# Kernel tuning notes

Measured on AMD Instinct MI355X. Metric: run time of the kernel, lower is better.

## Reference

```python
import jax, jax.numpy as jnp
import numpy as np

BIG = 1e10  # sentinel for geodesic-style padding in min/max morphology


def _cross_neighbors(x, pad_val):
    # x: [B,1,H,W]; gather center + 4-connected neighbors (cross structuring element)
    xp = jnp.pad(x, ((0, 0), (0, 0), (1, 1), (1, 1)), constant_values=pad_val)
    c = xp[:, :, 1:-1, 1:-1]
    u = xp[:, :, :-2, 1:-1]
    d = xp[:, :, 2:, 1:-1]
    l = xp[:, :, 1:-1, :-2]
    r = xp[:, :, 1:-1, 2:]
    return jnp.stack([c, u, d, l, r], axis=0)  # [5,B,1,H,W]


def opening_cross(x):
    # morphology opening = dilation(erosion(x)) with binary cross kernel
    er = jnp.min(_cross_neighbors(x, BIG), axis=0)
    return jnp.max(_cross_neighbors(er, -BIG), axis=0)


def torch_norm(x):
    mn = jnp.min(x)
    mx = jnp.max(x)
    return (x - mn) / (mx - mn + 1e-10)


def binarize(x):
    return jnp.where(x >= 0.5, jnp.float32(1.0), jnp.float32(0.0))


def connected_components(mask, num_iterations=150):
    # kornia.contrib.connected_components: init labels = flat pixel index on
    # foreground, then iterate 3x3 max-pool label propagation restricted to mask.
    B, C, H, W = mask.shape
    init = jnp.arange(B * C * H * W, dtype=jnp.float32).reshape(B, C, H, W) * mask
    fg = mask != 0

    def maxpool3(x):
        return jax.lax.reduce_window(
            x, -jnp.inf, jax.lax.max,
            window_dimensions=(1, 1, 3, 3), window_strides=(1, 1, 1, 1),
            padding='SAME')

    def body(i, out):
        return jnp.where(fg, maxpool3(out), out)

    return jax.lax.fori_loop(0, num_iterations, body, init)


def count_unique(x):
    # jit-compatible torch.unique(...).size()[0]: sort then count transitions.
    # Label values <= B*H*W < 2^24 so float32 comparisons are exact.
    s = jnp.sort(x.reshape(-1))
    return jnp.float32(1.0) + jnp.sum(s[1:] != s[:-1]).astype(jnp.float32)


def setup_inputs() -> dict:
    key = jax.random.key(0)
    k1, k2 = jax.random.split(key)
    img = jax.random.uniform(k1, (4, 1, 1024, 1024), dtype=jnp.float32)
    lab = jax.random.uniform(k2, (4, 1, 1024, 1024), dtype=jnp.float32)
    return {"img": img, "lab": lab}


def reference(img, lab):
    img = binarize(torch_norm(opening_cross(img)))
    lab = binarize(torch_norm(opening_cross(lab)))
    ccs = count_unique(connected_components(img, 150))
    ccsg = count_unique(connected_components(lab, 150))
    numSg = jnp.sum(lab)  # count_nonzero of binary mask
    C = jnp.abs(ccsg - ccs) / numSg
    return jnp.mean(C)
```

## Files before the change

kernel.cpp:

```cpp
#include <hip/hip_runtime.h>
#include <stdint.h>

#define WW 1024
#define HH 1024
#define NB 4
#define HW (HH * WW)
#define NPIX (NB * HW)
#define NT 4096
#define INVALID 0xFFFFFFFFu
#define RS 8


__device__ __forceinline__ void do_open_strip(const float* __restrict__ in,
                                              float* __restrict__ out,
                                              int strip, uint32_t* S,
                                              float2* __restrict__ mmslot) {
    int b  = strip >> 7;
    int y0 = (strip & 127) * RS;
    int t  = threadIdx.x;
    float* sx = (float*)S;
    float* sw = (float*)S + 2580;
    float* smin = (float*)S + 5160;
    float* smax = (float*)S + 5164;
    const float4* inb = (const float4*)(in + (size_t)b * HW);
    float4* outb      = (float4*)(out + (size_t)b * HW);

    float4 A[RS + 4];
    #pragma unroll
    for (int j = 0; j < RS + 4; j++) {
        int iy = y0 - 2 + j;
        if (iy >= 0 && iy < HH) A[j] = inb[iy * 256 + t];
        else A[j] = make_float4(1e10f, 1e10f, 1e10f, 1e10f);
    }
    #pragma unroll
    for (int rr = 0; rr < RS + 2; rr++) { sx[rr * 258 + t + 1] = A[rr + 1].x; sw[rr * 258 + t + 1] = A[rr + 1].w; }
    if (t < RS + 2) { sw[t * 258 + 0] = 1e10f; sx[t * 258 + 257] = 1e10f; }
    __syncthreads();

    float4 E[RS + 2];
    #pragma unroll
    for (int rr = 0; rr < RS + 2; rr++) {
        int ey = y0 - 1 + rr;
        float lw = sw[rr * 258 + t], rw = sx[rr * 258 + t + 2];
        float4 v = A[rr + 1];
        float hx = fminf(fminf(lw, v.x), v.y);
        float hy = fminf(fminf(v.x, v.y), v.z);
        float hz = fminf(fminf(v.y, v.z), v.w);
        float hw = fminf(fminf(v.z, v.w), rw);
        float4 e;
        e.x = fminf(hx, fminf(A[rr].x, A[rr + 2].x));
        e.y = fminf(hy, fminf(A[rr].y, A[rr + 2].y));
        e.z = fminf(hz, fminf(A[rr].z, A[rr + 2].z));
        e.w = fminf(hw, fminf(A[rr].w, A[rr + 2].w));
        if (ey < 0 || ey >= HH) e = make_float4(-1e10f, -1e10f, -1e10f, -1e10f);
        E[rr] = e;
    }
    __syncthreads();

    #pragma unroll
    for (int d = 0; d < RS; d++) { sx[d * 258 + t + 1] = E[d + 1].x; sw[d * 258 + t + 1] = E[d + 1].w; }
    if (t < RS) { sw[t * 258 + 0] = -1e10f; sx[t * 258 + 257] = -1e10f; }
    __syncthreads();

    float lmin = __uint_as_float(0x7F800000u);
    float lmax = 0.0f;
    #pragma unroll
    for (int d = 0; d < RS; d++) {
        float lw = sw[d * 258 + t], rw = sx[d * 258 + t + 2];
        float4 v = E[d + 1];
        float hx = fmaxf(fmaxf(lw, v.x), v.y);
        float hy = fmaxf(fmaxf(v.x, v.y), v.z);
        float hz = fmaxf(fmaxf(v.y, v.z), v.w);
        float hw = fmaxf(fmaxf(v.z, v.w), rw);
        float4 o;
        o.x = fmaxf(hx, fmaxf(E[d].x, E[d + 2].x));
        o.y = fmaxf(hy, fmaxf(E[d].y, E[d + 2].y));
        o.z = fmaxf(hz, fmaxf(E[d].z, E[d + 2].z));
        o.w = fmaxf(hw, fmaxf(E[d].w, E[d + 2].w));
        outb[(y0 + d) * 256 + t] = o;
        lmin = fminf(lmin, fminf(fminf(o.x, o.y), fminf(o.z, o.w)));
        lmax = fmaxf(lmax, fmaxf(fmaxf(o.x, o.y), fmaxf(o.z, o.w)));
    }
    for (int off = 32; off > 0; off >>= 1) {
        lmin = fminf(lmin, __shfl_down(lmin, off));
        lmax = fmaxf(lmax, __shfl_down(lmax, off));
    }
    if ((t & 63) == 0) { smin[t >> 6] = lmin; smax[t >> 6] = lmax; }
    __syncthreads();
    if (t == 0) {
        float m0 = fminf(fminf(smin[0], smin[1]), fminf(smin[2], smin[3]));
        float m1 = fmaxf(fmaxf(smax[0], smax[1]), fmaxf(smax[2], smax[3]));
        *mmslot = make_float2(m0, m1);
    }
}

__device__ __forceinline__ float calc_thr(float mn, float mx) {
    float denom = (mx - mn) + 1e-10f;
    uint32_t lo = 0, hi = 0x7F800000u;
    while (lo < hi) {
        uint32_t mid = (lo + hi) >> 1;
        float q = (__uint_as_float(mid) - mn) / denom;
        if (q >= 0.5f) hi = mid; else lo = mid + 1;
    }
    return __uint_as_float(lo);
}

__device__ __forceinline__ uint32_t lload(uint32_t* lp, uint32_t x) {
    return __hip_atomic_load(&lp[x], __ATOMIC_RELAXED, __HIP_MEMORY_SCOPE_WORKGROUP);
}
__device__ __forceinline__ uint32_t lfind(uint32_t* lp, uint32_t x) {
    uint32_t p = lload(lp, x);
    while (p != x) {
        uint32_t gp = lload(lp, p);
        if (gp != p)
            __hip_atomic_store(&lp[x], gp, __ATOMIC_RELAXED, __HIP_MEMORY_SCOPE_WORKGROUP);
        x = p; p = gp;
    }
    return x;
}
__device__ uint32_t lunion(uint32_t* lp, uint32_t a, uint32_t b) {
    uint32_t ra = lfind(lp, a), rb = lfind(lp, b);
    while (ra != rb) {
        uint32_t hi = ra > rb ? ra : rb;
        uint32_t lo = ra ^ rb ^ hi;
        uint32_t old = atomicCAS(&lp[lo], lo, hi);
        if (old == lo) return 1;
        ra = lfind(lp, old);
        rb = lfind(lp, hi);
    }
    return 0;
}
__device__ __forceinline__ int run_len(uint32_t bits) {
    return (int)__builtin_ctzll(~(uint64_t)bits);
}

__device__ void do_ccl_tile(const float* __restrict__ opened, uint8_t* __restrict__ desc,
                            uint32_t* __restrict__ parent, uint32_t* __restrict__ zt,
                            int bank, int tile, int L,
                            uint32_t* M, uint32_t* LP, uint32_t* SM,
                            float thr, uint32_t* pkslot) {
    int b  = tile >> 10;
    int tt = tile & 1023;
    int ty0 = (tt >> 5) << 5;
    int tx0 = (tt & 31) << 5;
    uint32_t base = (uint32_t)b * HW + (uint32_t)ty0 * WW + tx0;

    #pragma unroll
    for (int q = 0; q < 2; q++) {
        uint32_t u = (uint32_t)L + 64u * q;
        ((uint4*)LP)[u] = make_uint4(4*u, 4*u+1, 4*u+2, 4*u+3);
        ((uint4*)SM)[u] = make_uint4(INVALID, INVALID, INVALID, INVALID);
    }

    int r8 = L >> 3, c8 = (L & 7) << 2;
    uint32_t fgcnt = 0;
    #pragma unroll
    for (int q = 0; q < 4; q++) {
        int rr = r8 + 8 * q;
        float4 v = *(const float4*)(opened + base + (uint32_t)rr * WW + c8);
        uint32_t pb = (v.x >= thr ? 1u : 0u) | (v.y >= thr ? 2u : 0u)
                    | (v.z >= thr ? 4u : 0u) | (v.w >= thr ? 8u : 0u);
        fgcnt += __popc(pb);
        uint32_t part = pb << c8;
        part |= __shfl_xor(part, 1, 8);
        part |= __shfl_xor(part, 2, 8);
        part |= __shfl_xor(part, 4, 8);
        if ((L & 7) == 0) M[rr] = part;
    }
    __syncthreads();

    int r = L >> 1, h = L & 1;
    uint32_t rowm = M[r];
    uint32_t fstarts = rowm & ~(rowm << 1);
    uint32_t halfsel = 0xFFFFu << (16 * h);
    uint32_t starts = fstarts & halfsel;
    uint32_t runs = __popc(starts);
    uint32_t links = 0;
    if (r > 0 && starts) {
        uint32_t up = M[r - 1];
        uint32_t upstarts = up & ~(up << 1);
        uint32_t w0 = starts;
        while (w0) {
            int lx = __builtin_ctz(w0); w0 &= w0 - 1;
            int e = lx + run_len(rowm >> lx) - 1;
            int lo = lx ? lx - 1 : 0;
            int hi = (e >= 31) ? 31 : e + 1;
            uint32_t hm = (hi == 31) ? 0xFFFFFFFFu : ((1u << (hi + 1)) - 1u);
            uint32_t w = up & hm & ~((1u << lo) - 1u);
            uint32_t repA = ((uint32_t)r << 4) + __popc(fstarts & ((2u << e) - 1u)) - 1u;
            while (w) {
                int xs = __builtin_ctz(w);
                int xe = xs + run_len(up >> xs) - 1;
                uint32_t repB = (((uint32_t)r - 1) << 4)
                              + __popc(upstarts & ((2u << xe) - 1u)) - 1u;
                links += lunion(LP, repA, repB);
                w = (xe >= 31) ? 0u : (w & ~((1u << (xe + 1)) - 1u));
            }
        }
    }
    __syncthreads();

    if (tile == 0 && L == 0)
        zt[bank] = ((rowm & 1u) && !(rowm & 2u) && LP[0] == 0u) ? 1u : 0u;

    uint32_t rk[2]; bool fgk[2];
    #pragma unroll
    for (int j = 0; j < 2; j++) {
        int k = 2 * L + j;
        int li = (k < 32) ? k
               : (k < 64) ? (31 * 32 + (k - 32))
               : (k < 96) ? ((k - 64) << 5)
                          : (((k - 96) << 5) + 31);
        int ly = li >> 5, lx = li & 31;
        uint32_t rm = M[ly];
        bool f = (rm >> lx) & 1u;
        fgk[j] = f;
        if (f) {
            int e = lx + run_len(rm >> lx) - 1;
            uint32_t rst = rm & ~(rm << 1);
            uint32_t lbl = ((uint32_t)ly << 4) + __popc(rst & ((2u << e) - 1u)) - 1u;
            rk[j] = lfind(LP, lbl);
            atomicMin(&SM[rk[j]], (uint32_t)k);
        }
    }
    __syncthreads();

    uint32_t nodebase = (uint32_t)tile << 7;
    uint32_t d2 = 0;
    #pragma unroll
    for (int j = 0; j < 2; j++) {
        int k = 2 * L + j;
        uint32_t sb = 0xFFu;
        if (fgk[j]) {
            uint32_t s = SM[rk[j]];
            sb = s;
            if (s == (uint32_t)k) parent[nodebase + k] = nodebase + k;
        }
        d2 |= sb << (8 * j);
    }
    ((uint16_t*)desc)[((uint32_t)tile << 6) + L] = (uint16_t)d2;

    uint32_t pk = (fgcnt << 20) | (runs << 10) | links;
    for (int off = 32; off > 0; off >>= 1) pk += __shfl_down(pk, off);
    if (L == 0) *pkslot = pk;
    __syncthreads();
}

__device__ __forceinline__ uint32_t pload(uint32_t* P, uint32_t x) {
    return __hip_atomic_load(&P[x], __ATOMIC_RELAXED, __HIP_MEMORY_SCOPE_AGENT);
}
__device__ __forceinline__ uint32_t uf_find(uint32_t* P, uint32_t x) {
    uint32_t p = pload(P, x);
    while (p != x) {
        uint32_t gp = pload(P, p);
        if (gp != p)
            __hip_atomic_store(&P[x], gp, __ATOMIC_RELAXED, __HIP_MEMORY_SCOPE_AGENT);
        x = p; p = gp;
    }
    return x;
}
__device__ uint32_t uf_union(uint32_t* P, uint32_t a, uint32_t b) {
    uint32_t ra = uf_find(P, a);
    uint32_t rb = uf_find(P, b);
    while (ra != rb) {
        uint32_t hi = ra > rb ? ra : rb;
        uint32_t lo = ra ^ rb ^ hi;
        uint32_t old = atomicCAS(&P[lo], lo, hi);
        if (old == lo) return 1;
        ra = uf_find(P, old);
        rb = uf_find(P, hi);
    }
    return 0;
}

__global__ void k_open2(const float* __restrict__ img, const float* __restrict__ lab,
                        float* __restrict__ op0, float* __restrict__ op1,
                        float2* __restrict__ mm) {
    __shared__ uint32_t S[5168];
    int bank = blockIdx.x >> 9;
    do_open_strip(bank ? lab : img, bank ? op1 : op0,
                  blockIdx.x & 511, S, &mm[blockIdx.x]);
}

__global__ __launch_bounds__(256, 8) void k_ccl2(const float* __restrict__ op0,
                                                 const float* __restrict__ op1,
                                                 uint8_t* __restrict__ d0,
                                                 uint8_t* __restrict__ d1,
                                                 uint32_t* __restrict__ p0,
                                                 uint32_t* __restrict__ p1,
                                                 const float2* __restrict__ mm,
                                                 unsigned long long* __restrict__ fcs,
                                                 uint32_t* __restrict__ zt) {
    __shared__ uint32_t S[4240];
    int bank = blockIdx.x >> 10;
    int wave = threadIdx.x >> 6, L = threadIdx.x & 63;
    if (blockIdx.x == 0 && threadIdx.x == 0) zt[2] = 0;
    {
        const float2* mb = mm + (bank << 9);
        float2 u = mb[threadIdx.x];
        float2 v = mb[threadIdx.x + 256];
        float mn = fminf(u.x, v.x), mx = fmaxf(u.y, v.y);
        for (int off = 32; off > 0; off >>= 1) {
            mn = fminf(mn, __shfl_down(mn, off));
            mx = fmaxf(mx, __shfl_down(mx, off));
        }
        float* sf = (float*)(S + 4228);
        if (L == 0) { sf[wave] = mn; sf[4 + wave] = mx; }
    }
    __syncthreads();
    float* sf = (float*)(S + 4228);
    float mnA = fminf(fminf(sf[0], sf[1]), fminf(sf[2], sf[3]));
    float mxA = fmaxf(fmaxf(sf[4], sf[5]), fmaxf(sf[6], sf[7]));
    float thr = calc_thr(mnA, mxA);
    uint32_t* M = S + wave * 1056;
    int tile = ((blockIdx.x & 1023) << 2) + wave;
    do_ccl_tile(bank ? op1 : op0, bank ? d1 : d0, bank ? p1 : p0, zt, bank,
                tile, L, M, M + 32, M + 544, thr, &S[4224 + wave]);
    if (threadIdx.x == 0) {
        uint32_t fg = 0, comp = 0;
        #pragma unroll
        for (int w = 0; w < 4; w++) {
            uint32_t pk = S[4224 + w];
            fg   += pk >> 20;
            comp += ((pk >> 10) & 1023u) - (pk & 1023u);
        }
        fcs[blockIdx.x] = ((unsigned long long)comp << 32) | fg;
    }
}

__global__ __launch_bounds__(256) void k_border(const uint8_t* __restrict__ desc0,
                                                const uint8_t* __restrict__ desc1,
                                                uint32_t* __restrict__ parent0,
                                                uint32_t* __restrict__ parent1,
                                                unsigned long long* __restrict__ fcs,
                                                uint32_t* __restrict__ lks,
                                                uint32_t* __restrict__ zt,
                                                float* __restrict__ out) {
    __shared__ unsigned long long Q[800];
    __shared__ uint32_t qn;
    __shared__ uint32_t SW[6];
    __shared__ unsigned long long SB[8];
    __shared__ uint32_t SL[8];
    int inb  = blockIdx.x >> 10;
    int wave = threadIdx.x >> 6, L = threadIdx.x & 63;
    int tile = ((blockIdx.x & 1023) << 2) + wave;
    const uint8_t* desc = inb ? desc1 : desc0;
    uint32_t* parent = inb ? parent1 : parent0;

    if (threadIdx.x == 0) qn = 0;
    __syncthreads();

    {
        int tt = tile & 1023;
        int tyy = tt >> 5, txx = tt & 31;
        const uint8_t* dT = desc + ((uint32_t)tile << 7);
        uint32_t nT = (uint32_t)tile << 7;

        bool east  = (L < 32);
        int  x     = L & 31;
        bool valid = east ? (txx < 31) : (tyy < 31);
        int  tP    = east ? (tile + 1) : (tile + 32);
        uint32_t nP = (uint32_t)tP << 7;
        uint32_t sA = (uint32_t)dT[(east ? 96 : 32) + x];
        const uint8_t* dP = desc + (((uint32_t)tP << 7) + (east ? 64u : 0u));
        uint32_t t = valid ? (uint32_t)dP[x] : 0xFFu;

        uint32_t tp1  = __shfl(t,  L + 1);
        uint32_t tm1  = __shfl(t,  L - 1);
        uint32_t sAp1 = __shfl(sA, L + 1);
        uint32_t sAm1 = __shfl(sA, L - 1);

        if (valid && sA != 0xFFu) {
            uint32_t a = nT + sA;
            if (t != 0xFFu && !(x > 0 && sAm1 == sA && tm1 == t)) {
                uint32_t i = atomicAdd(&qn, 1u);
                Q[i] = ((unsigned long long)a << 32) | (nP + t);
            }
            if (x < 31 && tp1 != 0xFFu && tp1 != t && sAp1 != sA) {
                uint32_t i = atomicAdd(&qn, 1u);
                Q[i] = ((unsigned long long)a << 32) | (nP + tp1);
            }
            if (x > 0 && tm1 != 0xFFu && tm1 != t && sAm1 != sA) {
                uint32_t i = atomicAdd(&qn, 1u);
                Q[i] = ((unsigned long long)a << 32) | (nP + tm1);
            }
        }
        if (L == 0 && tyy < 31 && txx < 31) {
            int tSE = tile + 33;
            uint32_t sB = dT[63];
            uint32_t sQ = desc[((uint32_t)tSE << 7)];
            if (sB != 0xFFu && sQ != 0xFFu) {
                uint32_t i = atomicAdd(&qn, 1u);
                Q[i] = ((unsigned long long)(nT + sB) << 32) | (((uint32_t)tSE << 7) + sQ);
            }
        }
        if (L == 1 && tyy < 31 && txx > 0) {
            int tSW = tile + 31;
            uint32_t sB = dT[32];
            uint32_t sQ = desc[((uint32_t)tSW << 7) + 31];
            if (sB != 0xFFu && sQ != 0xFFu) {
                uint32_t i = atomicAdd(&qn, 1u);
                Q[i] = ((unsigned long long)(nT + sB) << 32) | (((uint32_t)tSW << 7) + sQ);
            }
        }
    }
    __syncthreads();

    uint32_t n = qn;
    uint32_t links = 0;
    for (uint32_t i = threadIdx.x; i < n; i += 256) {
        unsigned long long q = Q[i];
        links += uf_union(parent, (uint32_t)(q >> 32), (uint32_t)q);
    }

    for (int off = 32; off > 0; off >>= 1) links += __shfl_down(links, off);
    if (L == 0) SW[wave] = links;
    __syncthreads();
    if (threadIdx.x == 0) {
        uint32_t lk = SW[0] + SW[1] + SW[2] + SW[3];
        __hip_atomic_store(&lks[blockIdx.x], lk, __ATOMIC_RELAXED, __HIP_MEMORY_SCOPE_AGENT);
        asm volatile("s_waitcnt vmcnt(0)" ::: "memory");
        uint32_t old = __hip_atomic_fetch_add(&zt[2], 1u,
                                              __ATOMIC_RELAXED, __HIP_MEMORY_SCOPE_AGENT);
        SW[4] = old;
    }
    __syncthreads();
    if (SW[4] == 2047u) {
        unsigned long long a0 = 0, a1 = 0;
        uint32_t l0 = 0, l1 = 0;
        #pragma unroll
        for (int k = 0; k < 4; k++) {
            int i = (int)threadIdx.x + (k << 8);
            a0 += __hip_atomic_load(&fcs[i],        __ATOMIC_RELAXED, __HIP_MEMORY_SCOPE_AGENT);
            a1 += __hip_atomic_load(&fcs[1024 + i], __ATOMIC_RELAXED, __HIP_MEMORY_SCOPE_AGENT);
            l0 += __hip_atomic_load(&lks[i],        __ATOMIC_RELAXED, __HIP_MEMORY_SCOPE_AGENT);
            l1 += __hip_atomic_load(&lks[1024 + i], __ATOMIC_RELAXED, __HIP_MEMORY_SCOPE_AGENT);
        }
        for (int off = 32; off > 0; off >>= 1) {
            a0 += __shfl_down(a0, off);
            a1 += __shfl_down(a1, off);
            l0 += __shfl_down(l0, off);
            l1 += __shfl_down(l1, off);
        }
        if (L == 0) { SB[wave] = a0; SB[4 + wave] = a1; SL[wave] = l0; SL[4 + wave] = l1; }
        __syncthreads();
        if (threadIdx.x == 0) {
            unsigned long long A0 = SB[0] + SB[1] + SB[2] + SB[3];
            unsigned long long A1 = SB[4] + SB[5] + SB[6] + SB[7];
            uint32_t gl0 = SL[0] + SL[1] + SL[2] + SL[3];
            uint32_t gl1 = SL[4] + SL[5] + SL[6] + SL[7];
            uint32_t nf0 = (uint32_t)A0, lc0 = (uint32_t)(A0 >> 32);
            uint32_t nf1 = (uint32_t)A1, lc1 = (uint32_t)(A1 >> 32);
            uint32_t z0 = __hip_atomic_load(&zt[0], __ATOMIC_RELAXED, __HIP_MEMORY_SCOPE_AGENT);
            uint32_t z1 = __hip_atomic_load(&zt[1], __ATOMIC_RELAXED, __HIP_MEMORY_SCOPE_AGENT);
            uint32_t comps0 = lc0 - gl0;
            uint32_t comps1 = lc1 - gl1;
            float ccs  = (float)(comps0 - z0 + ((nf0 < (uint32_t)NPIX || z0) ? 1u : 0u));
            float ccsg = (float)(comps1 - z1 + ((nf1 < (uint32_t)NPIX || z1) ? 1u : 0u));
            out[0] = fabsf(ccsg - ccs) / (float)nf1;
        }
    }
}

extern "C" void kernel_launch(void* const* d_in, const int* in_sizes, int n_in,
                              void* d_out, int out_size, void* d_ws, size_t ws_size,
                              hipStream_t stream) {
    const float* img = (const float*)d_in[0];
    const float* lab = (const float*)d_in[1];
    float* out = (float*)d_out;
    char* ws = (char*)d_ws;

    float*    op0 = (float*)ws;
    float*    op1 = (float*)(ws + (size_t)16 * 1024 * 1024);
    uint8_t*  d0  = (uint8_t*)(ws + (size_t)32 * 1024 * 1024);
    uint8_t*  d1  = (uint8_t*)(ws + (size_t)32 * 1024 * 1024 + 512 * 1024);
    uint32_t* p0  = (uint32_t*)(ws + (size_t)33 * 1024 * 1024);
    uint32_t* p1  = (uint32_t*)(ws + (size_t)35 * 1024 * 1024);
    char*     aux = ws + (size_t)37 * 1024 * 1024;
    float2*   mm  = (float2*)aux;
    unsigned long long* fcs = (unsigned long long*)(aux + 8192);
    uint32_t* lks = (uint32_t*)(aux + 24576);
    uint32_t* zt  = (uint32_t*)(aux + 32768);

    k_open2<<<2 * NB * (HH / RS), 256, 0, stream>>>(img, lab, op0, op1, mm);
    k_ccl2<<<2 * NT / 4, 256, 0, stream>>>(op0, op1, d0, d1, p0, p1, mm, fcs, zt);
    k_border<<<2 * NT / 4, 256, 0, stream>>>(d0, d1, p0, p1, fcs, lks, zt, out);
}
```

Baseline: 130.5 us.

## Fuse border union-find into CCL kernel using per-seam atomic handshake

Drops the separate border kernel and merges tile-boundary merging into the local CCL kernel. Each block publishes tags on the seams it shares with neighbouring blocks using atomic exchanges keyed by a per-launch nonce. The second block to reach a seam processes the cross-tile links for it, so border unions start without waiting for a grid-wide kernel boundary. This removes one launch and the tail of a kernel, at the cost of more atomics, relaxed-ordering subtleties, and uneven work per block.

```diff
diff --git a/kernel.cpp b/kernel.cpp
--- a/kernel.cpp
+++ b/kernel.cpp
@@ -10,6 +10,20 @@
 #define INVALID 0xFFFFFFFFu
 #define RS 8
 
+
+__device__ __forceinline__ uint32_t aload32(const uint32_t* p) {
+    return __hip_atomic_load(p, __ATOMIC_RELAXED, __HIP_MEMORY_SCOPE_AGENT);
+}
+__device__ __forceinline__ void astore32(uint32_t* p, uint32_t v) {
+    __hip_atomic_store(p, v, __ATOMIC_RELAXED, __HIP_MEMORY_SCOPE_AGENT);
+}
+__device__ __forceinline__ unsigned long long ctag(uint32_t word, uint32_t side,
+                                                   uint32_t nonce) {
+    unsigned long long x = ((unsigned long long)nonce << 24)
+                         ^ ((unsigned long long)word * 2u + side)
+                         ^ 0xA5C3000000000000ull;
+    return x * 0x9E3779B97F4A7C15ull + 0x0123456789ABCDEFull;
+}
 
 __device__ __forceinline__ void do_open_strip(const float* __restrict__ in,
                                               float* __restrict__ out,
@@ -201,7 +215,7 @@
     __syncthreads();
 
     if (tile == 0 && L == 0)
-        zt[bank] = ((rowm & 1u) && !(rowm & 2u) && LP[0] == 0u) ? 1u : 0u;
+        astore32(&zt[bank], ((rowm & 1u) && !(rowm & 2u) && LP[0] == 0u) ? 1u : 0u);
 
     uint32_t rk[2]; bool fgk[2];
     #pragma unroll
@@ -234,11 +248,14 @@
         if (fgk[j]) {
             uint32_t s = SM[rk[j]];
             sb = s;
-            if (s == (uint32_t)k) parent[nodebase + k] = nodebase + k;
+            if (s == (uint32_t)k)
+                astore32(&parent[nodebase + k], nodebase + k);
         }
         d2 |= sb << (8 * j);
     }
-    ((uint16_t*)desc)[((uint32_t)tile << 6) + L] = (uint16_t)d2;
+    uint32_t w2 = d2 | (__shfl_down(d2, 1) << 16);
+    if ((L & 1) == 0)
+        astore32((uint32_t*)desc + (((uint32_t)tile) << 5) + (L >> 1), w2);
 
     uint32_t pk = (fgcnt << 20) | (runs << 10) | links;
     for (int off = 32; off > 0; off >>= 1) pk += __shfl_down(pk, off);
@@ -275,26 +292,38 @@
 
 __global__ void k_open2(const float* __restrict__ img, const float* __restrict__ lab,
                         float* __restrict__ op0, float* __restrict__ op1,
-                        float2* __restrict__ mm) {
+                        float2* __restrict__ mm, uint32_t* __restrict__ zt) {
     __shared__ uint32_t S[5168];
+    if (blockIdx.x == 0 && threadIdx.x == 0) {
+        astore32(&zt[2], 0u);
+        uint32_t n = __hip_atomic_fetch_add(&zt[3], 1u,
+                                            __ATOMIC_RELAXED, __HIP_MEMORY_SCOPE_AGENT);
+        astore32(&zt[4], n);
+    }
     int bank = blockIdx.x >> 9;
     do_open_strip(bank ? lab : img, bank ? op1 : op0,
                   blockIdx.x & 511, S, &mm[blockIdx.x]);
 }
 
-__global__ __launch_bounds__(256, 8) void k_ccl2(const float* __restrict__ op0,
-                                                 const float* __restrict__ op1,
-                                                 uint8_t* __restrict__ d0,
-                                                 uint8_t* __restrict__ d1,
-                                                 uint32_t* __restrict__ p0,
-                                                 uint32_t* __restrict__ p1,
-                                                 const float2* __restrict__ mm,
-                                                 unsigned long long* __restrict__ fcs,
-                                                 uint32_t* __restrict__ zt) {
-    __shared__ uint32_t S[4240];
+__global__ __launch_bounds__(256, 8) void k_cclb(
+        const float* __restrict__ op0, const float* __restrict__ op1,
+        uint8_t* __restrict__ d0, uint8_t* __restrict__ d1,
+        uint32_t* __restrict__ p0, uint32_t* __restrict__ p1,
+        const float2* __restrict__ mm,
+        unsigned long long* __restrict__ fcs, uint32_t* __restrict__ lks,
+        unsigned long long* __restrict__ cw, uint32_t* __restrict__ zt,
+        float* __restrict__ out) {
+    __shared__ __align__(16) uint32_t S[4240];
+    __shared__ uint32_t wonA[8], slist[16], clist[16], nsc2[2], qn;
+    __shared__ uint32_t SWK[6];
+    __shared__ unsigned long long SB[8];
+    __shared__ uint32_t SL[8];
+
     int bank = blockIdx.x >> 10;
     int wave = threadIdx.x >> 6, L = threadIdx.x & 63;
-    if (blockIdx.x == 0 && threadIdx.x == 0) zt[2] = 0;
+    uint8_t* desc = bank ? d1 : d0;
+    uint32_t* parent = bank ? p1 : p0;
+
     {
         const float2* mb = mm + (bank << 9);
         float2 u = mb[threadIdx.x];
@@ -312,9 +341,10 @@
     float mnA = fminf(fminf(sf[0], sf[1]), fminf(sf[2], sf[3]));
     float mxA = fmaxf(fmaxf(sf[4], sf[5]), fmaxf(sf[6], sf[7]));
     float thr = calc_thr(mnA, mxA);
+
     uint32_t* M = S + wave * 1056;
     int tile = ((blockIdx.x & 1023) << 2) + wave;
-    do_ccl_tile(bank ? op1 : op0, bank ? d1 : d0, bank ? p1 : p0, zt, bank,
+    do_ccl_tile(bank ? op1 : op0, desc, parent, zt, bank,
                 tile, L, M, M + 32, M + 544, thr, &S[4224 + wave]);
     if (threadIdx.x == 0) {
         uint32_t fg = 0, comp = 0;
@@ -324,85 +354,115 @@
             fg   += pk >> 20;
             comp += ((pk >> 10) & 1023u) - (pk & 1023u);
         }
-        fcs[blockIdx.x] = ((unsigned long long)comp << 32) | fg;
-    }
-}
-
-__global__ __launch_bounds__(256) void k_border(const uint8_t* __restrict__ desc0,
-                                                const uint8_t* __restrict__ desc1,
-                                                uint32_t* __restrict__ parent0,
-                                                uint32_t* __restrict__ parent1,
-                                                unsigned long long* __restrict__ fcs,
-                                                uint32_t* __restrict__ lks,
-                                                uint32_t* __restrict__ zt,
-                                                float* __restrict__ out) {
-    __shared__ unsigned long long Q[800];
-    __shared__ uint32_t qn;
-    __shared__ uint32_t SW[6];
-    __shared__ unsigned long long SB[8];
-    __shared__ uint32_t SL[8];
-    int inb  = blockIdx.x >> 10;
-    int wave = threadIdx.x >> 6, L = threadIdx.x & 63;
-    int tile = ((blockIdx.x & 1023) << 2) + wave;
-    const uint8_t* desc = inb ? desc1 : desc0;
-    uint32_t* parent = inb ? parent1 : parent0;
-
-    if (threadIdx.x == 0) qn = 0;
-    __syncthreads();
-
-    {
-        int tt = tile & 1023;
-        int tyy = tt >> 5, txx = tt & 31;
-        const uint8_t* dT = desc + ((uint32_t)tile << 7);
-        uint32_t nT = (uint32_t)tile << 7;
-
-        bool east  = (L < 32);
-        int  x     = L & 31;
-        bool valid = east ? (txx < 31) : (tyy < 31);
-        int  tP    = east ? (tile + 1) : (tile + 32);
-        uint32_t nP = (uint32_t)tP << 7;
-        uint32_t sA = (uint32_t)dT[(east ? 96 : 32) + x];
-        const uint8_t* dP = desc + (((uint32_t)tP << 7) + (east ? 64u : 0u));
-        uint32_t t = valid ? (uint32_t)dP[x] : 0xFFu;
-
+        __hip_atomic_store(&fcs[blockIdx.x],
+                           ((unsigned long long)comp << 32) | fg,
+                           __ATOMIC_RELAXED, __HIP_MEMORY_SCOPE_AGENT);
+    }
+
+    if (threadIdx.x < 8) {
+        int j = threadIdx.x & 3;
+        bool fw = threadIdx.x < 4;
+        int k = (j == 0) ? 1 : (j == 1) ? 7 : (j == 2) ? 8 : 9;
+        long long A = fw ? (long long)blockIdx.x : (long long)blockIdx.x - k;
+        uint32_t won = 0xFFFFFFFFu;
+        if (A >= 0) {
+            uint32_t Ar = (uint32_t)A;
+            uint32_t a255 = Ar & 255u, a7 = Ar & 7u;
+            bool valid = (k == 1) ? (a7 != 7u)
+                       : (k == 7) ? ((a255 < 248u) && (a7 != 0u))
+                       : (k == 8) ? (a255 < 248u)
+                                  : ((a255 < 248u) && (a7 != 7u));
+            if (valid) {
+                uint32_t nonce = aload32(&zt[4]);
+                uint32_t word = Ar * 4u + (uint32_t)j;
+                unsigned long long my = ctag(word, fw ? 0u : 1u, nonce);
+                unsigned long long ot = ctag(word, fw ? 1u : 0u, nonce);
+                unsigned long long old = __hip_atomic_exchange(&cw[word], my,
+                        __ATOMIC_RELAXED, __HIP_MEMORY_SCOPE_AGENT);
+                if (old == ot) won = Ar;
+            }
+        }
+        wonA[threadIdx.x] = won;
+    }
+    if (threadIdx.x == 200) qn = 0;
+    __syncthreads();
+
+    if (threadIdx.x == 0) {
+        int ns = 0, nc = 0;
+        uint32_t tb = (blockIdx.x & 1023u) << 2;
+        slist[ns++] = tb + 0;
+        slist[ns++] = tb + 1;
+        slist[ns++] = tb + 2;
+        #pragma unroll
+        for (int s = 0; s < 8; s++) {
+            uint32_t A = wonA[s];
+            if (A == 0xFFFFFFFFu) continue;
+            uint32_t at = (A & 1023u) << 2;
+            int j = s & 3;
+            if (j == 0) slist[ns++] = at + 3;
+            else if (j == 2) {
+                slist[ns++] = (at + 0) | 0x1000u;
+                slist[ns++] = (at + 1) | 0x1000u;
+                slist[ns++] = (at + 2) | 0x1000u;
+                slist[ns++] = (at + 3) | 0x1000u;
+                clist[nc++] = at + 0;  clist[nc++] = at + 1;  clist[nc++] = at + 2;
+                clist[nc++] = (at + 1) | 0x1000u;  clist[nc++] = (at + 2) | 0x1000u;
+                clist[nc++] = (at + 3) | 0x1000u;
+            }
+            else if (j == 3) clist[nc++] = at + 3;
+            else clist[nc++] = at | 0x1000u;
+        }
+        nsc2[0] = (uint32_t)ns; nsc2[1] = (uint32_t)nc;
+    }
+    __syncthreads();
+
+    unsigned long long* Q = (unsigned long long*)S;
+    uint32_t ns = nsc2[0], nc = nsc2[1];
+    const uint32_t* d32 = (const uint32_t*)desc;
+    for (uint32_t s0 = 0; s0 < ns; s0 += 8) {
+        uint32_t s = s0 + (threadIdx.x >> 5);
+        int x = threadIdx.x & 31;
+        uint32_t sA = 0xFFu, t = 0xFFu, nQ = 0, nP = 0;
+        bool act = (s < ns);
+        if (act) {
+            uint32_t e = slist[s];
+            uint32_t Qt = e & 4095u;
+            bool row = (e & 0x1000u) != 0;
+            uint32_t Pt = row ? (Qt + 32u) : (Qt + 1u);
+            nQ = Qt << 7; nP = Pt << 7;
+            uint32_t ob = row ? (32u + (uint32_t)x) : (96u + (uint32_t)x);
+            uint32_t wA = aload32(d32 + (Qt << 5) + (ob >> 2));
+            sA = (wA >> ((ob & 3u) * 8u)) & 0xFFu;
+            uint32_t pb = row ? (uint32_t)x : (64u + (uint32_t)x);
+            uint32_t wB = aload32(d32 + (Pt << 5) + (pb >> 2));
+            t = (wB >> ((pb & 3u) * 8u)) & 0xFFu;
+        }
         uint32_t tp1  = __shfl(t,  L + 1);
         uint32_t tm1  = __shfl(t,  L - 1);
         uint32_t sAp1 = __shfl(sA, L + 1);
         uint32_t sAm1 = __shfl(sA, L - 1);
-
-        if (valid && sA != 0xFFu) {
-            uint32_t a = nT + sA;
-            if (t != 0xFFu && !(x > 0 && sAm1 == sA && tm1 == t)) {
-                uint32_t i = atomicAdd(&qn, 1u);
-                Q[i] = ((unsigned long long)a << 32) | (nP + t);
-            }
-            if (x < 31 && tp1 != 0xFFu && tp1 != t && sAp1 != sA) {
-                uint32_t i = atomicAdd(&qn, 1u);
-                Q[i] = ((unsigned long long)a << 32) | (nP + tp1);
-            }
-            if (x > 0 && tm1 != 0xFFu && tm1 != t && sAm1 != sA) {
-                uint32_t i = atomicAdd(&qn, 1u);
-                Q[i] = ((unsigned long long)a << 32) | (nP + tm1);
-            }
-        }
-        if (L == 0 && tyy < 31 && txx < 31) {
-            int tSE = tile + 33;
-            uint32_t sB = dT[63];
-            uint32_t sQ = desc[((uint32_t)tSE << 7)];
-            if (sB != 0xFFu && sQ != 0xFFu) {
-                uint32_t i = atomicAdd(&qn, 1u);
-                Q[i] = ((unsigned long long)(nT + sB) << 32) | (((uint32_t)tSE << 7) + sQ);
-            }
-        }
-        if (L == 1 && tyy < 31 && txx > 0) {
-            int tSW = tile + 31;
-            uint32_t sB = dT[32];
-            uint32_t sQ = desc[((uint32_t)tSW << 7) + 31];
-            if (sB != 0xFFu && sQ != 0xFFu) {
-                uint32_t i = atomicAdd(&qn, 1u);
-                Q[i] = ((unsigned long long)(nT + sB) << 32) | (((uint32_t)tSW << 7) + sQ);
-            }
-        }
+        if (act && sA != 0xFFu) {
+            uint32_t a = nQ + sA;
+            if (t != 0xFFu && !(x > 0 && sAm1 == sA && tm1 == t))
+                Q[atomicAdd(&qn, 1u)] = ((unsigned long long)a << 32) | (nP + t);
+            if (x < 31 && tp1 != 0xFFu && tp1 != t && sAp1 != sA)
+                Q[atomicAdd(&qn, 1u)] = ((unsigned long long)a << 32) | (nP + tp1);
+            if (x > 0 && tm1 != 0xFFu && tm1 != t && sAm1 != sA)
+                Q[atomicAdd(&qn, 1u)] = ((unsigned long long)a << 32) | (nP + tm1);
+        }
+    }
+    if (threadIdx.x < nc) {
+        uint32_t e = clist[threadIdx.x];
+        uint32_t Qt = e & 4095u;
+        bool isSW = (e & 0x1000u) != 0;
+        uint32_t Pt = isSW ? (Qt + 31u) : (Qt + 33u);
+        uint32_t wA = aload32(d32 + (Qt << 5) + (isSW ? 8u : 15u));
+        uint32_t sB = isSW ? (wA & 0xFFu) : ((wA >> 24) & 0xFFu);
+        uint32_t wB = aload32(d32 + (Pt << 5) + (isSW ? 7u : 0u));
+        uint32_t sQ = isSW ? ((wB >> 24) & 0xFFu) : (wB & 0xFFu);
+        if (sB != 0xFFu && sQ != 0xFFu)
+            Q[atomicAdd(&qn, 1u)] =
+                ((unsigned long long)((Qt << 7) + sB) << 32) | ((Pt << 7) + sQ);
     }
     __syncthreads();
 
@@ -412,20 +472,19 @@
         unsigned long long q = Q[i];
         links += uf_union(parent, (uint32_t)(q >> 32), (uint32_t)q);
     }
-
     for (int off = 32; off > 0; off >>= 1) links += __shfl_down(links, off);
-    if (L == 0) SW[wave] = links;
+    if (L == 0) SWK[wave] = links;
     __syncthreads();
     if (threadIdx.x == 0) {
-        uint32_t lk = SW[0] + SW[1] + SW[2] + SW[3];
+        uint32_t lk = SWK[0] + SWK[1] + SWK[2] + SWK[3];
         __hip_atomic_store(&lks[blockIdx.x], lk, __ATOMIC_RELAXED, __HIP_MEMORY_SCOPE_AGENT);
         asm volatile("s_waitcnt vmcnt(0)" ::: "memory");
         uint32_t old = __hip_atomic_fetch_add(&zt[2], 1u,
                                               __ATOMIC_RELAXED, __HIP_MEMORY_SCOPE_AGENT);
-        SW[4] = old;
-    }
-    __syncthreads();
-    if (SW[4] == 2047u) {
+        SWK[4] = old;
+    }
+    __syncthreads();
+    if (SWK[4] == 2047u) {
         unsigned long long a0 = 0, a1 = 0;
         uint32_t l0 = 0, l1 = 0;
         #pragma unroll
@@ -433,8 +492,8 @@
             int i = (int)threadIdx.x + (k << 8);
             a0 += __hip_atomic_load(&fcs[i],        __ATOMIC_RELAXED, __HIP_MEMORY_SCOPE_AGENT);
             a1 += __hip_atomic_load(&fcs[1024 + i], __ATOMIC_RELAXED, __HIP_MEMORY_SCOPE_AGENT);
-            l0 += __hip_atomic_load(&lks[i],        __ATOMIC_RELAXED, __HIP_MEMORY_SCOPE_AGENT);
-            l1 += __hip_atomic_load(&lks[1024 + i], __ATOMIC_RELAXED, __HIP_MEMORY_SCOPE_AGENT);
+            l0 += aload32(&lks[i]);
+            l1 += aload32(&lks[1024 + i]);
         }
         for (int off = 32; off > 0; off >>= 1) {
             a0 += __shfl_down(a0, off);
@@ -451,8 +510,8 @@
             uint32_t gl1 = SL[4] + SL[5] + SL[6] + SL[7];
             uint32_t nf0 = (uint32_t)A0, lc0 = (uint32_t)(A0 >> 32);
             uint32_t nf1 = (uint32_t)A1, lc1 = (uint32_t)(A1 >> 32);
-            uint32_t z0 = __hip_atomic_load(&zt[0], __ATOMIC_RELAXED, __HIP_MEMORY_SCOPE_AGENT);
-            uint32_t z1 = __hip_atomic_load(&zt[1], __ATOMIC_RELAXED, __HIP_MEMORY_SCOPE_AGENT);
+            uint32_t z0 = aload32(&zt[0]);
+            uint32_t z1 = aload32(&zt[1]);
             uint32_t comps0 = lc0 - gl0;
             uint32_t comps1 = lc1 - gl1;
             float ccs  = (float)(comps0 - z0 + ((nf0 < (uint32_t)NPIX || z0) ? 1u : 0u));
@@ -481,8 +540,9 @@
     unsigned long long* fcs = (unsigned long long*)(aux + 8192);
     uint32_t* lks = (uint32_t*)(aux + 24576);
     uint32_t* zt  = (uint32_t*)(aux + 32768);
-
-    k_open2<<<2 * NB * (HH / RS), 256, 0, stream>>>(img, lab, op0, op1, mm);
-    k_ccl2<<<2 * NT / 4, 256, 0, stream>>>(op0, op1, d0, d1, p0, p1, mm, fcs, zt);
-    k_border<<<2 * NT / 4, 256, 0, stream>>>(d0, d1, p0, p1, fcs, lks, zt, out);
-}
+    unsigned long long* cw  = (unsigned long long*)(aux + 40960);
+
+    k_open2<<<2 * NB * (HH / RS), 256, 0, stream>>>(img, lab, op0, op1, mm, zt);
+    k_cclb<<<2 * NT / 4, 256, 0, stream>>>(op0, op1, d0, d1, p0, p1, mm,
+                                           fcs, lks, cw, zt, out);
+}
```

Result: slower. 134.6 us (+3.2%).
